# Kernel optimization log

Hardware: AMD Instinct MI355X
Metric: run time of the kernel (lower is better)

## Reference

```python
import math
import jax, jax.numpy as jnp
import numpy as np

GROUPS = 32
EPS = 1e-5


def group_norm(x, gamma, beta):
    # x: (b, c, h, w); normalize per-group over (c/g, h, w)
    b, c, h, w = x.shape
    xg = x.reshape(b, GROUPS, c // GROUPS, h, w)
    mu = xg.mean(axis=(2, 3, 4), keepdims=True)
    var = xg.var(axis=(2, 3, 4), keepdims=True)
    xn = ((xg - mu) * jax.lax.rsqrt(var + EPS)).reshape(b, c, h, w)
    return xn * gamma[None, :, None, None] + beta[None, :, None, None]


def conv1x1(x, w, bias):
    # x: (b, c, h, w), w: (o, c) -> (b, o, h, w)
    return jnp.einsum('bchw,oc->bohw', x, w) + bias[None, :, None, None]


def setup_inputs() -> dict:
    key = jax.random.key(0)
    ks = jax.random.split(key, 7)
    b, c, h, w = 8, 512, 32, 32
    s = 1.0 / math.sqrt(c)
    return {
        'x': jax.random.normal(ks[0], (b, c, h, w), dtype=jnp.float32),
        'gn_w': jnp.ones((c,), dtype=jnp.float32),
        'gn_b': jnp.zeros((c,), dtype=jnp.float32),
        'qkv_w': jax.random.normal(ks[1], (3 * c, c), dtype=jnp.float32) * s,
        'qkv_b': jnp.zeros((3 * c,), dtype=jnp.float32),
        'proj_w': jax.random.normal(ks[2], (c, c), dtype=jnp.float32) * s,
        'proj_b': jnp.zeros((c,), dtype=jnp.float32),
        'num_heads': 8,
    }


def reference(x, gn_w, gn_b, qkv_w, qkv_b, proj_w, proj_b, num_heads):
    b, c, h, w = x.shape
    hds = num_heads
    d = c // hds
    x_ = group_norm(x, gn_w, gn_b)
    qkv = conv1x1(x_, qkv_w, qkv_b)  # (b, 3c, h, w)
    q, k, v = jnp.split(qkv, 3, axis=1)
    # (b, hds, d, hw)
    q = q.reshape(b, hds, d, h * w)
    k = k.reshape(b, hds, d, h * w)
    v = v.reshape(b, hds, d, h * w)
    # scores: (b, hds, hw, hw) = q^T k / sqrt(d)
    scores = jnp.einsum('bhdq,bhdk->bhqk', q, k) / math.sqrt(d)
    attn = jax.nn.softmax(scores, axis=-1)
    # out = (attn @ v^T)^T -> (b, hds, d, hw)
    out = jnp.einsum('bhqk,bhdk->bhdq', attn, v)
    out = out.reshape(b, c, h, w)
    return x + conv1x1(out, proj_w, proj_b)
```

## Files before the change

### kernel.cpp

```cpp
#include <hip/hip_runtime.h>


typedef __attribute__((ext_vector_type(8))) short short8v;
typedef __attribute__((ext_vector_type(4))) short short4v;
typedef __attribute__((ext_vector_type(4))) float f32x4;
typedef __attribute__((ext_vector_type(2))) unsigned uint2v;
typedef __attribute__((ext_vector_type(4))) unsigned uint4v;

constexpr int Bn = 8, Cn = 512, HWn = 1024;

#if __has_builtin(__builtin_amdgcn_exp2f)
#define EXP2F(x) __builtin_amdgcn_exp2f(x)
#else
#define EXP2F(x) __exp2f(x)
#endif

static __device__ __forceinline__ short bf16_of(float f) {
  union { float f; unsigned u; } v{f};
  unsigned r = v.u + 0x7fffu + ((v.u >> 16) & 1u);
  return (short)(r >> 16);
}
static __device__ __forceinline__ unsigned bf16pk(float a, float b) {
  return (unsigned)(unsigned short)bf16_of(a) |
         ((unsigned)(unsigned short)bf16_of(b) << 16);
}

static __device__ __forceinline__ void gload16(const void* g, void* l) {
  __builtin_amdgcn_global_load_lds(
      (const __attribute__((address_space(1))) unsigned*)g,
      (__attribute__((address_space(3))) unsigned*)l, 16, 0, 0);
}

__global__ __launch_bounds__(256) void gn_fused_k(const float* __restrict__ x,
                                                  const float* __restrict__ gw,
                                                  const float* __restrict__ gb,
                                                  const float* __restrict__ wq,
                                                  const float* __restrict__ wp,
                                                  short* __restrict__ oq,
                                                  short* __restrict__ op,
                                                  short* __restrict__ xn3) {
  const int t = threadIdx.x;
  if (blockIdx.x >= 256) {
    int i = (blockIdx.x - 256) * 256 + t;
    const float* src = wq;
    short* dst = oq;
    int idx = i;
    if (i >= 196608) { src = wp; dst = op; idx = i - 196608; }
    f32x4 v = ((const f32x4*)src)[idx];
    short4v o;
    o.x = bf16_of(v.x); o.y = bf16_of(v.y); o.z = bf16_of(v.z); o.w = bf16_of(v.w);
    *(short4v*)&dst[idx * 4] = o;
    return;
  }
  const int bg = blockIdx.x;
  const int g = bg & 31;
  const f32x4* src = (const f32x4*)(x + (size_t)bg * 16384);
  f32x4 v[16];
  float s = 0.f, ss = 0.f;
#pragma unroll
  for (int k = 0; k < 16; k++) {
    v[k] = src[t + 256 * k];
    s += v[k].x + v[k].y + v[k].z + v[k].w;
    ss += v[k].x * v[k].x + v[k].y * v[k].y + v[k].z * v[k].z + v[k].w * v[k].w;
  }
#pragma unroll
  for (int off = 32; off; off >>= 1) {
    s += __shfl_xor(s, off);
    ss += __shfl_xor(ss, off);
  }
  __shared__ float rs[4], rss[4];
  const int lane = t & 63, w = t >> 6;
  if (lane == 0) { rs[w] = s; rss[w] = ss; }
  __syncthreads();
  const float S = rs[0] + rs[1] + rs[2] + rs[3];
  const float SS = rss[0] + rss[1] + rss[2] + rss[3];
  constexpr float invn = 1.0f / 16384.f;
  const float mu = S * invn;
  const float var = SS * invn - mu * mu;
  const float rstd = rsqrtf(var + 1e-5f);
  float ga[16], be[16];
#pragma unroll
  for (int k = 0; k < 16; k++) {
    ga[k] = gw[g * 16 + k] * rstd;
    be[k] = gb[g * 16 + k] - mu * ga[k];
  }
  short* dst = xn3 + (size_t)bg * 16384;
#pragma unroll
  for (int d = 0; d < 4; d++) {
    unsigned pk[8];
#pragma unroll
    for (int k = 0; k < 16; k += 2)
      pk[k >> 1] = bf16pk(fmaf(v[k][d], ga[k], be[k]),
                          fmaf(v[k + 1][d], ga[k + 1], be[k + 1]));
    uint4v lo = {pk[0], pk[1], pk[2], pk[3]};
    uint4v hi = {pk[4], pk[5], pk[6], pk[7]};
    *(uint4v*)&dst[(4 * t + d) * 16] = lo;
    *(uint4v*)&dst[(4 * t + d) * 16 + 8] = hi;
  }
}

__device__ __forceinline__ short8v frag64(const short* buf, int row, int gk) {
  return *(const short8v*)&buf[row * 64 + ((gk ^ (row & 7)) << 3)];
}
__device__ __forceinline__ short8v frag128(const short* buf, int row, int gk) {
  return *(const short8v*)&buf[row * 128 + ((gk ^ (row & 7)) << 3)];
}

__global__ __launch_bounds__(256, 2) void gemm_qkv_k(
    const short* __restrict__ A, const short* __restrict__ xn3,
    const float* __restrict__ bias, short* __restrict__ oQ,
    short* __restrict__ oK, short* __restrict__ oV) {
  const int bid = blockIdx.x;
  const int swz = (bid & 7) * 96 + (bid >> 3);
  const int bn = swz & 7;
  const int rest = swz >> 3;
  const int bm = rest % 12, b = rest / 12;
  const bool VBLK = (bm >= 8);

  const short* Bb = xn3 + (size_t)b * 524288;
  __shared__ __align__(16) short As[128 * 64];
  __shared__ __align__(16) short Bs[128 * 64];
  const int t = threadIdx.x, l = t & 63, w = t >> 6;
  const int wr = w >> 1, wc = w & 1;
  const int m0 = bm * 128, n0 = bn * 128;
  const f32x4 vzero = {0.f, 0.f, 0.f, 0.f};
  f32x4 acc[4][4];
#pragma unroll
  for (int i = 0; i < 4; i++)
#pragma unroll
    for (int j = 0; j < 4; j++) acc[i][j] = vzero;

  const int sr0 = t >> 3;
  const int sg = t & 7;

  for (int k0 = 0; k0 < 512; k0 += 64) {
#pragma unroll
    for (int it = 0; it < 4; it++) {
      int r = it * 32 + sr0;
      int gs = sg ^ (r & 7);
      gload16(&A[(size_t)(m0 + r) * 512 + k0 + gs * 8], &As[it * 2048 + w * 512]);
      int gp = (k0 >> 4) + (gs >> 1);
      gload16(&Bb[(size_t)((gp << 10) + n0 + r) * 16 + ((gs & 1) << 3)],
              &Bs[it * 2048 + w * 512]);
    }
    __syncthreads();
#pragma unroll
    for (int kk = 0; kk < 2; kk++) {
      short8v af[4], bf[4];
#pragma unroll
      for (int i = 0; i < 4; i++)
        af[i] = frag64(As, wr * 64 + i * 16 + (l & 15), kk * 4 + (l >> 4));
#pragma unroll
      for (int j = 0; j < 4; j++)
        bf[j] = frag64(Bs, wc * 64 + j * 16 + (l & 15), kk * 4 + (l >> 4));
      if (VBLK) {
#pragma unroll
        for (int i = 0; i < 4; i++)
#pragma unroll
          for (int j = 0; j < 4; j++)
            acc[i][j] = __builtin_amdgcn_mfma_f32_16x16x32_bf16(bf[j], af[i], acc[i][j], 0, 0, 0);
      } else {
#pragma unroll
        for (int i = 0; i < 4; i++)
#pragma unroll
          for (int j = 0; j < 4; j++)
            acc[i][j] = __builtin_amdgcn_mfma_f32_16x16x32_bf16(af[i], bf[j], acc[i][j], 0, 0, 0);
      }
    }
    __syncthreads();
  }

  if (!VBLK) {
    short* oBase = (m0 < 512) ? oQ : oK;
    const int mc = (m0 < 512 ? m0 : m0 - 512) + wr * 64;
#pragma unroll
    for (int i = 0; i < 4; i++) {
      int mi = mc + i * 16 + (l >> 4) * 4;
      f32x4 bv = *(const f32x4*)&bias[m0 + wr * 64 + i * 16 + (l >> 4) * 4];
#pragma unroll
      for (int j = 0; j < 4; j++) {
        int n = n0 + wc * 64 + j * 16 + (l & 15);
        uint2v pk = {bf16pk(acc[i][j][0] + bv[0], acc[i][j][1] + bv[1]),
                     bf16pk(acc[i][j][2] + bv[2], acc[i][j][3] + bv[3])};
        *(uint2v*)&oBase[((size_t)b * HWn + n) * 512 + mi] = pk;
      }
    }
  } else {
#pragma unroll
    for (int i = 0; i < 4; i++) {
      int m = m0 + wr * 64 + i * 16 + (l & 15);
      float bv = bias[m];
      short* vrow = oV + ((size_t)b * 512 + (m - 1024)) * HWn;
#pragma unroll
      for (int j = 0; j < 4; j++) {
        int n = n0 + wc * 64 + j * 16 + (l >> 4) * 4;
        uint2v pk = {bf16pk(acc[i][j][0] + bv, acc[i][j][1] + bv),
                     bf16pk(acc[i][j][2] + bv, acc[i][j][3] + bv)};
        *(uint2v*)&vrow[n] = pk;
      }
    }
  }
}

__global__ __launch_bounds__(512, 2) void gemm_proj_k(
    const short* __restrict__ A, const short* __restrict__ Bt,
    const float* __restrict__ bias, const float* __restrict__ resid,
    float* __restrict__ outF) {
  const int bid = blockIdx.x;
  const int swz = (bid & 7) * 32 + (bid >> 3);
  const int bn = swz & 7;
  const int rest = swz >> 3;
  const int bm = rest & 3, b = rest >> 2;

  const short* Bb = Bt + (size_t)b * HWn * Cn;
  __shared__ __align__(16) short As[128 * 64];
  __shared__ __align__(16) short Bs[128 * 64];
  const int t = threadIdx.x, l = t & 63, w = t >> 6;
  const int wr = w >> 1, wc = w & 1;
  const int m0 = bm * 128, n0 = bn * 128;
  const f32x4 vzero = {0.f, 0.f, 0.f, 0.f};
  f32x4 acc[2][4];
#pragma unroll
  for (int i = 0; i < 2; i++)
#pragma unroll
    for (int j = 0; j < 4; j++) acc[i][j] = vzero;

  const int sr0 = t >> 3;
  const int sg = t & 7;

  for (int k0 = 0; k0 < 512; k0 += 64) {
#pragma unroll
    for (int it = 0; it < 2; it++) {
      int r = it * 64 + sr0;
      int gs = sg ^ (r & 7);
      gload16(&A[(size_t)(m0 + r) * 512 + k0 + gs * 8], &As[it * 4096 + w * 512]);
      gload16(&Bb[(size_t)(n0 + r) * 512 + k0 + gs * 8], &Bs[it * 4096 + w * 512]);
    }
    __syncthreads();
#pragma unroll
    for (int kk = 0; kk < 2; kk++) {
      short8v af[2], bf[4];
#pragma unroll
      for (int i = 0; i < 2; i++)
        af[i] = frag64(As, wr * 32 + i * 16 + (l & 15), kk * 4 + (l >> 4));
#pragma unroll
      for (int j = 0; j < 4; j++)
        bf[j] = frag64(Bs, wc * 64 + j * 16 + (l & 15), kk * 4 + (l >> 4));
#pragma unroll
      for (int i = 0; i < 2; i++)
#pragma unroll
        for (int j = 0; j < 4; j++)
          acc[i][j] = __builtin_amdgcn_mfma_f32_16x16x32_bf16(af[i], bf[j], acc[i][j], 0, 0, 0);
    }
    __syncthreads();
  }

  float* outb = outF + (size_t)b * Cn * HWn;
  const float* rb = resid + (size_t)b * Cn * HWn;
#pragma unroll
  for (int i = 0; i < 2; i++) {
    f32x4 bv = *(const f32x4*)&bias[m0 + wr * 32 + i * 16 + (l >> 4) * 4];
#pragma unroll
    for (int r = 0; r < 4; r++) {
      int m = m0 + wr * 32 + i * 16 + (l >> 4) * 4 + r;
#pragma unroll
      for (int j = 0; j < 4; j++) {
        int n = n0 + wc * 64 + j * 16 + (l & 15);
        size_t idx = (size_t)m * HWn + n;
        outb[idx] = acc[i][j][r] + bv[r] + rb[idx];
      }
    }
  }
}

__global__ __launch_bounds__(256, 2) void attn_k(const short* __restrict__ qT,
                                                 const short* __restrict__ kT,
                                                 const short* __restrict__ vB,
                                                 short* __restrict__ aoT) {
  const int bid = blockIdx.x;
  const int swz = (bid & 7) * 64 + (bid >> 3);
  const int qt = swz & 7, head = (swz >> 3) & 7, b = swz >> 6;
  __shared__ __align__(16) short SM[33792];
  short* Ks = SM;
  short* Vs = SM + 8192;
  short* Ps = SM + 16384;
  const int t = threadIdx.x, l = t & 63, w = t >> 6;
  short* PsA = Ps + (2 * w) * 2176;
  short* PsB = Ps + (2 * w + 1) * 2176;
  const int g = l >> 4;
  const f32x4 vzero = {0.f, 0.f, 0.f, 0.f};

  const short* ksrc = kT + (size_t)b * HWn * 512 + head * 64;
  const short* vsrc = vB + ((size_t)b * 512 + head * 64) * HWn;

  const short* qbase = qT +
      ((size_t)b * HWn + qt * 128 + 32 * w + (l & 15)) * 512 + head * 64 + g * 8;
  const short8v qA0 = *(const short8v*)&qbase[0];
  const short8v qA1 = *(const short8v*)&qbase[32];
  const short8v qB0 = *(const short8v*)&qbase[16 * 512];
  const short8v qB1 = *(const short8v*)&qbase[16 * 512 + 32];

  const int kkv0 = w * 8 + (l >> 3), kg = l & 7;
  const int vd0 = w * 4 + (l >> 4), vg = l & 15;

#pragma unroll
  for (int it = 0; it < 4; it++) {
    int kv = kkv0 + it * 32;
    gload16(&ksrc[(size_t)kv * 512 + (kg ^ (kv & 7)) * 8], &Ks[it * 2048 + w * 512]);
    int d = vd0 + it * 16;
    gload16(&vsrc[(size_t)d * HWn + (vg ^ (d & 7)) * 8], &Vs[it * 2048 + w * 512]);
  }
  __syncthreads();

  f32x4 oaA[4], oaB[4];
#pragma unroll
  for (int f = 0; f < 4; f++) { oaA[f] = vzero; oaB[f] = vzero; }
  float lA = 0.f, lB = 0.f;
  constexpr float SC = 0.1803368801111f;
  constexpr float MOFF = -11.5415602855f;

#pragma unroll 1
  for (int kt = 0; kt < 8; kt++) {
    short8v kreg[4], vreg[4];
    if (kt < 7) {
      const int kt1 = kt + 1;
#pragma unroll
      for (int it = 0; it < 4; it++) {
        int kv = kkv0 + it * 32;
        kreg[it] = *(const short8v*)&ksrc[(size_t)(kt1 * 128 + kv) * 512 +
                                          (kg ^ (kv & 7)) * 8];
        int d = vd0 + it * 16;
        vreg[it] = *(const short8v*)&vsrc[(size_t)d * HWn + kt1 * 128 +
                                          (vg ^ (d & 7)) * 8];
      }
    }

    f32x4 saA[8], saB[8];
    __builtin_amdgcn_s_setprio(1);
#pragma unroll
    for (int f = 0; f < 8; f++) {
      short8v ka0 = frag64(Ks, 16 * f + (l & 15), g);
      short8v ka1 = frag64(Ks, 16 * f + (l & 15), g + 4);
      saA[f] = __builtin_amdgcn_mfma_f32_16x16x32_bf16(ka0, qA0, vzero, 0, 0, 0);
      saB[f] = __builtin_amdgcn_mfma_f32_16x16x32_bf16(ka0, qB0, vzero, 0, 0, 0);
      saA[f] = __builtin_amdgcn_mfma_f32_16x16x32_bf16(ka1, qA1, saA[f], 0, 0, 0);
      saB[f] = __builtin_amdgcn_mfma_f32_16x16x32_bf16(ka1, qB1, saB[f], 0, 0, 0);
    }
    __builtin_amdgcn_s_setprio(0);

    float psA = 0.f, psB = 0.f;
#pragma unroll
    for (int f = 0; f < 8; f++)
#pragma unroll
      for (int r = 0; r < 4; r++) {
        float eA = EXP2F(fmaf(saA[f][r], SC, MOFF));
        float eB = EXP2F(fmaf(saB[f][r], SC, MOFF));
        saA[f][r] = eA;
        saB[f][r] = eB;
        psA += eA;
        psB += eB;
      }
    psA += __shfl_xor(psA, 16);
    psA += __shfl_xor(psA, 32);
    psB += __shfl_xor(psB, 16);
    psB += __shfl_xor(psB, 32);
    lA += psA;
    lB += psB;

#pragma unroll
    for (int f = 0; f < 8; f++) {
      int o = (l & 15) * 136 + 16 * f + 4 * g;
      uint2v pkA = {bf16pk(saA[f][0], saA[f][1]), bf16pk(saA[f][2], saA[f][3])};
      uint2v pkB = {bf16pk(saB[f][0], saB[f][1]), bf16pk(saB[f][2], saB[f][3])};
      *(uint2v*)&PsA[o] = pkA;
      *(uint2v*)&PsB[o] = pkB;
    }
    short8v paA[4], paB[4];
#pragma unroll
    for (int c = 0; c < 4; c++) {
      paA[c] = *(const short8v*)&PsA[(l & 15) * 136 + c * 32 + g * 8];
      paB[c] = *(const short8v*)&PsB[(l & 15) * 136 + c * 32 + g * 8];
    }
    __builtin_amdgcn_s_setprio(1);
#pragma unroll
    for (int fd = 0; fd < 4; fd++) {
      int row = 16 * fd + (l & 15);
#pragma unroll
      for (int c = 0; c < 4; c++) {
        short8v vb = frag128(Vs, row, c * 4 + g);
        oaA[fd] = __builtin_amdgcn_mfma_f32_16x16x32_bf16(paA[c], vb, oaA[fd], 0, 0, 0);
        oaB[fd] = __builtin_amdgcn_mfma_f32_16x16x32_bf16(paB[c], vb, oaB[fd], 0, 0, 0);
      }
    }
    __builtin_amdgcn_s_setprio(0);

    if (kt < 7) {
      __syncthreads();
#pragma unroll
      for (int it = 0; it < 4; it++) {
        *(short8v*)&Ks[it * 2048 + w * 512 + l * 8] = kreg[it];
        *(short8v*)&Vs[it * 2048 + w * 512 + l * 8] = vreg[it];
      }
      __syncthreads();
    }
  }

  const float invA = 1.0f / lA, invB = 1.0f / lB;
  float ivA[4], ivB[4];
#pragma unroll
  for (int r = 0; r < 4; r++) {
    ivA[r] = __shfl(invA, 4 * g + r);
    ivB[r] = __shfl(invB, 4 * g + r);
  }
#pragma unroll
  for (int r = 0; r < 4; r++)
#pragma unroll
    for (int f = 0; f < 4; f++) {
      PsA[(4 * g + r) * 136 + 16 * f + (l & 15)] = bf16_of(oaA[f][r] * ivA[r]);
      PsB[(4 * g + r) * 136 + 16 * f + (l & 15)] = bf16_of(oaB[f][r] * ivB[r]);
    }
  __syncthreads();
  short* dst = aoT + ((size_t)b * HWn + qt * 128) * 512 + head * 64;
#pragma unroll
  for (int it = 0; it < 4; it++) {
    int r = (t >> 3) + 32 * it;
    int c8 = (t & 7) * 8;
    *(short8v*)&dst[(size_t)r * 512 + c8] =
        *(const short8v*)&Ps[(r >> 4) * 2176 + (r & 15) * 136 + c8];
  }
}

extern "C" void kernel_launch(void* const* d_in, const int* in_sizes, int n_in,
                              void* d_out, int out_size, void* d_ws, size_t ws_size,
                              hipStream_t stream) {
  const float* x = (const float*)d_in[0];
  const float* gn_w = (const float*)d_in[1];
  const float* gn_b = (const float*)d_in[2];
  const float* qkv_w = (const float*)d_in[3];
  const float* qkv_b = (const float*)d_in[4];
  const float* proj_w = (const float*)d_in[5];
  const float* proj_b = (const float*)d_in[6];
  float* out = (float*)d_out;

  char* ws = (char*)d_ws;
  short* wqb = (short*)(ws + 4096);
  short* wpb = (short*)(ws + 4096 + 1572864);
  char* p = ws + 4096 + 1572864 + 524288;
  const size_t SB = (size_t)Bn * HWn * 512 * 2;
  short* xn3 = (short*)p;
  short* qT = (short*)(p + SB);
  short* kT = (short*)(p + 2 * SB);
  short* vB = (short*)(p + 3 * SB);
  short* aoT = (short*)(p + 4 * SB);

  gn_fused_k<<<1280, 256, 0, stream>>>(x, gn_w, gn_b, qkv_w, proj_w, wqb, wpb, xn3);
  gemm_qkv_k<<<768, 256, 0, stream>>>(wqb, xn3, qkv_b, qT, kT, vB);
  attn_k<<<512, 256, 0, stream>>>(qT, kT, vB, aoT);
  gemm_proj_k<<<256, 512, 0, stream>>>(wpb, aoT, proj_b, x, out);
}
```

Before: 80.88 us.

## Double-buffer LDS in QKV and projection GEMMs; use native bf16 conversion

Both the QKV and the output-projection GEMMs now use two LDS buffers per operand. The global-to-LDS load of the next K-slice is issued before the MFMA work on the current slice, so one barrier per step both overlaps and protects the loads. The manual round-to-nearest-even bf16 conversion is swapped for the HIP __float2bfloat16 intrinsic. In the attention softmax the per-lane exp sum is split into four independent accumulators to shorten the dependency chain. The doubled LDS footprint (64KB per block) may limit occupancy, and the changed summation order slightly alters rounding.

```diff
diff --git a/kernel.cpp b/kernel.cpp
--- a/kernel.cpp
+++ b/kernel.cpp
@@ -1,4 +1,5 @@
 #include <hip/hip_runtime.h>
+#include <hip/hip_bf16.h>
 
 
 typedef __attribute__((ext_vector_type(8))) short short8v;
@@ -15,14 +16,15 @@
 #define EXP2F(x) __exp2f(x)
 #endif
 
+static __device__ __forceinline__ unsigned short bf16u(float f) {
+  __hip_bfloat16 h = __float2bfloat16(f);
+  return __builtin_bit_cast(unsigned short, h);
+}
 static __device__ __forceinline__ short bf16_of(float f) {
-  union { float f; unsigned u; } v{f};
-  unsigned r = v.u + 0x7fffu + ((v.u >> 16) & 1u);
-  return (short)(r >> 16);
+  return (short)bf16u(f);
 }
 static __device__ __forceinline__ unsigned bf16pk(float a, float b) {
-  return (unsigned)(unsigned short)bf16_of(a) |
-         ((unsigned)(unsigned short)bf16_of(b) << 16);
+  return (unsigned)bf16u(a) | ((unsigned)bf16u(b) << 16);
 }
 
 static __device__ __forceinline__ void gload16(const void* g, void* l) {
@@ -118,8 +120,8 @@
   const bool VBLK = (bm >= 8);
 
   const short* Bb = xn3 + (size_t)b * 524288;
-  __shared__ __align__(16) short As[128 * 64];
-  __shared__ __align__(16) short Bs[128 * 64];
+  __shared__ __align__(16) short As[2][8192];
+  __shared__ __align__(16) short Bs[2][8192];
   const int t = threadIdx.x, l = t & 63, w = t >> 6;
   const int wr = w >> 1, wc = w & 1;
   const int m0 = bm * 128, n0 = bn * 128;
@@ -133,26 +135,34 @@
   const int sr0 = t >> 3;
   const int sg = t & 7;
 
-  for (int k0 = 0; k0 < 512; k0 += 64) {
-#pragma unroll
-    for (int it = 0; it < 4; it++) {
-      int r = it * 32 + sr0;
-      int gs = sg ^ (r & 7);
-      gload16(&A[(size_t)(m0 + r) * 512 + k0 + gs * 8], &As[it * 2048 + w * 512]);
-      int gp = (k0 >> 4) + (gs >> 1);
-      gload16(&Bb[(size_t)((gp << 10) + n0 + r) * 16 + ((gs & 1) << 3)],
-              &Bs[it * 2048 + w * 512]);
-    }
-    __syncthreads();
+#define STAGE_QKV(buf, k0)                                                    \
+  do {                                                                        \
+    _Pragma("unroll") for (int it = 0; it < 4; it++) {                        \
+      int r = it * 32 + sr0;                                                  \
+      int gs = sg ^ (r & 7);                                                  \
+      gload16(&A[(size_t)(m0 + r) * 512 + (k0) + gs * 8],                     \
+              &As[buf][it * 2048 + w * 512]);                                 \
+      int gp = ((k0) >> 4) + (gs >> 1);                                       \
+      gload16(&Bb[(size_t)((gp << 10) + n0 + r) * 16 + ((gs & 1) << 3)],      \
+              &Bs[buf][it * 2048 + w * 512]);                                 \
+    }                                                                         \
+  } while (0)
+
+  STAGE_QKV(0, 0);
+  __syncthreads();
+
+  for (int ks = 0; ks < 8; ks++) {
+    const int cb = ks & 1;
+    if (ks < 7) STAGE_QKV(cb ^ 1, (ks + 1) * 64);
 #pragma unroll
     for (int kk = 0; kk < 2; kk++) {
       short8v af[4], bf[4];
 #pragma unroll
       for (int i = 0; i < 4; i++)
-        af[i] = frag64(As, wr * 64 + i * 16 + (l & 15), kk * 4 + (l >> 4));
+        af[i] = frag64(&As[cb][0], wr * 64 + i * 16 + (l & 15), kk * 4 + (l >> 4));
 #pragma unroll
       for (int j = 0; j < 4; j++)
-        bf[j] = frag64(Bs, wc * 64 + j * 16 + (l & 15), kk * 4 + (l >> 4));
+        bf[j] = frag64(&Bs[cb][0], wc * 64 + j * 16 + (l & 15), kk * 4 + (l >> 4));
       if (VBLK) {
 #pragma unroll
         for (int i = 0; i < 4; i++)
@@ -213,8 +223,8 @@
   const int bm = rest & 3, b = rest >> 2;
 
   const short* Bb = Bt + (size_t)b * HWn * Cn;
-  __shared__ __align__(16) short As[128 * 64];
-  __shared__ __align__(16) short Bs[128 * 64];
+  __shared__ __align__(16) short As[2][8192];
+  __shared__ __align__(16) short Bs[2][8192];
   const int t = threadIdx.x, l = t & 63, w = t >> 6;
   const int wr = w >> 1, wc = w & 1;
   const int m0 = bm * 128, n0 = bn * 128;
@@ -228,24 +238,33 @@
   const int sr0 = t >> 3;
   const int sg = t & 7;
 
-  for (int k0 = 0; k0 < 512; k0 += 64) {
-#pragma unroll
-    for (int it = 0; it < 2; it++) {
-      int r = it * 64 + sr0;
-      int gs = sg ^ (r & 7);
-      gload16(&A[(size_t)(m0 + r) * 512 + k0 + gs * 8], &As[it * 4096 + w * 512]);
-      gload16(&Bb[(size_t)(n0 + r) * 512 + k0 + gs * 8], &Bs[it * 4096 + w * 512]);
-    }
-    __syncthreads();
+#define STAGE_PROJ(buf, k0)                                                   \
+  do {                                                                        \
+    _Pragma("unroll") for (int it = 0; it < 2; it++) {                        \
+      int r = it * 64 + sr0;                                                  \
+      int gs = sg ^ (r & 7);                                                  \
+      gload16(&A[(size_t)(m0 + r) * 512 + (k0) + gs * 8],                     \
+              &As[buf][it * 4096 + w * 512]);                                 \
+      gload16(&Bb[(size_t)(n0 + r) * 512 + (k0) + gs * 8],                    \
+              &Bs[buf][it * 4096 + w * 512]);                                 \
+    }                                                                         \
+  } while (0)
+
+  STAGE_PROJ(0, 0);
+  __syncthreads();
+
+  for (int ks = 0; ks < 8; ks++) {
+    const int cb = ks & 1;
+    if (ks < 7) STAGE_PROJ(cb ^ 1, (ks + 1) * 64);
 #pragma unroll
     for (int kk = 0; kk < 2; kk++) {
       short8v af[2], bf[4];
 #pragma unroll
       for (int i = 0; i < 2; i++)
-        af[i] = frag64(As, wr * 32 + i * 16 + (l & 15), kk * 4 + (l >> 4));
+        af[i] = frag64(&As[cb][0], wr * 32 + i * 16 + (l & 15), kk * 4 + (l >> 4));
 #pragma unroll
       for (int j = 0; j < 4; j++)
-        bf[j] = frag64(Bs, wc * 64 + j * 16 + (l & 15), kk * 4 + (l >> 4));
+        bf[j] = frag64(&Bs[cb][0], wc * 64 + j * 16 + (l & 15), kk * 4 + (l >> 4));
 #pragma unroll
       for (int i = 0; i < 2; i++)
 #pragma unroll
@@ -348,7 +367,7 @@
     }
     __builtin_amdgcn_s_setprio(0);
 
-    float psA = 0.f, psB = 0.f;
+    f32x4 psAv = vzero, psBv = vzero;
 #pragma unroll
     for (int f = 0; f < 8; f++)
 #pragma unroll
@@ -357,9 +376,11 @@
         float eB = EXP2F(fmaf(saB[f][r], SC, MOFF));
         saA[f][r] = eA;
         saB[f][r] = eB;
-        psA += eA;
-        psB += eB;
-      }
+        psAv[r] += eA;
+        psBv[r] += eB;
+      }
+    float psA = (psAv[0] + psAv[1]) + (psAv[2] + psAv[3]);
+    float psB = (psBv[0] + psBv[1]) + (psBv[2] + psBv[3]);
     psA += __shfl_xor(psA, 16);
     psA += __shfl_xor(psA, 32);
     psB += __shfl_xor(psB, 16);
```

After: 79.94 us (median of 2 runs). Within noise of the previous version (-1.2%).
